# Kernel optimization log

Measured on AMD Instinct MI355X. Metric: run time of the kernel, lower is better.

## Reference

```python
import jax, jax.numpy as jnp
import numpy as np

HID = 1024
H = 8
HD = HID // H  # 128; KV length must equal HD for the bias-add broadcast
B = 8
LQ = 4096
LK = HD


def setup_inputs() -> dict:
    key = jax.random.key(0)
    ks = jax.random.split(key, 16)
    s = 0.02
    inp = {
        "query": jax.random.normal(ks[0], (B, LQ, HID), jnp.float32),
        "key": jax.random.normal(ks[1], (B, LK, HID), jnp.float32),
        "value": jax.random.normal(ks[2], (B, LK, HID), jnp.float32),
        "atten": jax.random.normal(ks[3], (B, LQ, HID), jnp.float32),
        "mask": jax.random.randint(ks[4], (B, 1, 1, LK), 0, 2, jnp.int32),
        "Wq": jax.random.normal(ks[5], (HID, HID), jnp.float32) * s,
        "bq": jnp.zeros((HID,), jnp.float32),
        "Wk": jax.random.normal(ks[6], (HID, HID), jnp.float32) * s,
        "bk": jnp.zeros((HID,), jnp.float32),
        "Wv": jax.random.normal(ks[7], (HID, HID), jnp.float32) * s,
        "bv": jnp.zeros((HID,), jnp.float32),
        "Watt": jax.random.normal(ks[8], (HID, HID), jnp.float32) * s,
        "batt": jnp.zeros((HID,), jnp.float32),
        "Wfc": jax.random.normal(ks[9], (HID, HID), jnp.float32) * s,
        "bfc": jnp.zeros((HID,), jnp.float32),
    }
    return inp


def _heads(x):
    # [B, L, HID] -> [B, H, L, HD]
    b, l, _ = x.shape
    return x.reshape(b, l, H, HD).transpose(0, 2, 1, 3)


def reference(query, key, value, atten, mask, Wq, bq, Wk, bk, Wv, bv, Watt, batt, Wfc, bfc):
    scale = jnp.sqrt(jnp.asarray(HD, jnp.float32))
    atten_out = _heads(atten @ Watt.T + batt)          # [B,H,LQ,HD]
    Q = _heads(query @ Wq.T + bq)                      # [B,H,LQ,HD]
    K = _heads(key @ Wk.T + bk)                        # [B,H,LK,HD]
    V = _heads(value @ Wv.T + bv)                      # [B,H,LK,HD]
    energy = jnp.einsum('bhqd,bhkd->bhqk', Q, K) / scale + atten_out  # LK == HD
    energy = jnp.where(mask == 0, jnp.float32(-1e10), energy)
    attention = jax.nn.softmax(energy, axis=-1)
    x = jnp.einsum('bhqk,bhkd->bhqd', attention, V)
    x = x.transpose(0, 2, 1, 3).reshape(query.shape[0], -1, HID)
    return x @ Wfc.T + bfc
```

## Files before the change

### kernel.cpp

```cpp
#include <hip/hip_runtime.h>
#include <hip/hip_bf16.h>
#include <stdint.h>

typedef __bf16 bf16_t;
typedef __bf16 bf16x8 __attribute__((ext_vector_type(8)));
typedef __bf16 bf16x4 __attribute__((ext_vector_type(4)));
typedef float f32x4 __attribute__((ext_vector_type(4)));

#define HIDN 1024
#define NHEAD 8
#define HDIM 128
#define NBATCH 8
#define LQLEN 4096
#define LKLEN 128

__device__ __forceinline__ void gload_lds16(const void* g, void* l) {
  __builtin_amdgcn_global_load_lds(
      (const __attribute__((address_space(1))) unsigned int*)g,
      (__attribute__((address_space(3))) unsigned int*)l, 16, 0, 0);
}

__global__ __launch_bounds__(256) void convk(const float* __restrict__ in,
                                             bf16_t* __restrict__ out, int n4) {
  int i = blockIdx.x * blockDim.x + threadIdx.x;
  const int stride = gridDim.x * blockDim.x;
  for (; i < n4; i += stride) {
    const float4 v = ((const float4*)in)[i];
    bf16x4 o;
    o[0] = (bf16_t)v.x; o[1] = (bf16_t)v.y; o[2] = (bf16_t)v.z; o[3] = (bf16_t)v.w;
    ((bf16x4*)out)[i] = o;
  }
}

template <int MODE>
__global__ __launch_bounds__(512, 2) void gemm8p(const bf16_t* __restrict__ A,
                                                 const bf16_t* __restrict__ Bw,
                                                 const float* __restrict__ bias,
                                                 void* __restrict__ Cout) {
  constexpr int NT = 32;
  constexpr int SLOT = 32768;
  __shared__ uint4 smem_raw[8192];
  char* smem = (char*)smem_raw;

  const int tid = threadIdx.x;
  const int wid = tid >> 6, lane = tid & 63;
  const int lr = lane & 15, lh = lane >> 4;
  const int wr = wid >> 2, wc = wid & 3;

  const int bid = blockIdx.x;
  const int m_blk = (bid & 7) * 16 + (bid >> 5);
  const int n_blk = (bid >> 3) & 3;
  const int m0 = m_blk * 256, n0 = n_blk * 256;

  const int c0 = tid, c1 = tid + 512;
  const int sc0 = (((c0 & 3) ^ ((c0 >> 3) & 3)) << 4);
  const int sc1 = (((c1 & 3) ^ ((c1 >> 3) & 3)) << 4);
  const char* srcA0 = (const char*)A + (size_t)(m0 + (c0 >> 2)) * 2048 + sc0;
  const char* srcA1 = (const char*)A + (size_t)(m0 + (c1 >> 2)) * 2048 + sc1;
  const char* srcB0 = (const char*)Bw + (size_t)(n0 + (c0 >> 2)) * 2048 + sc0;
  const char* srcB1 = (const char*)Bw + (size_t)(n0 + (c1 >> 2)) * 2048 + sc1;
  const int d0 = c0 * 16, d1 = c1 * 16;

  f32x4 acc[8][4] = {};

#pragma unroll
  for (int tt = 0; tt < 3; ++tt) {
    char* dst = smem + tt * SLOT;
    gload_lds16(srcA0 + tt * 64, dst + d0);
    gload_lds16(srcA1 + tt * 64, dst + d1);
    gload_lds16(srcB0 + tt * 64, dst + 16384 + d0);
    gload_lds16(srcB1 + tt * 64, dst + 16384 + d1);
  }
  asm volatile("s_waitcnt vmcnt(8)" ::: "memory");
  __builtin_amdgcn_s_barrier();
  __builtin_amdgcn_sched_barrier(0);

  const int swz = ((lr >> 1) & 3) << 4;
  const int aoff = (wr * 128 + lr) * 64 + ((lh << 4) ^ swz);
  const int boff = 16384 + (wc * 64 + lr) * 64 + ((lh << 4) ^ swz);

  for (int t = 0; t < NT; ++t) {
    const char* sA = smem + (t & 3) * SLOT + aoff;
    const char* sB = smem + (t & 3) * SLOT + boff;
    char* dst = smem + ((t + 3) & 3) * SLOT;
    const int kb = (t + 3) * 64;
    const bool pf = (t <= NT - 4);

    bf16x8 bfr[4], af[8];
#pragma unroll
    for (int n = 0; n < 4; ++n) bfr[n] = *(const bf16x8*)(sB + n * 1024);
#pragma unroll
    for (int m = 0; m < 8; ++m) af[m] = *(const bf16x8*)(sA + m * 1024);
    if (pf) {
      gload_lds16(srcA0 + kb, dst + d0);
      gload_lds16(srcA1 + kb, dst + d1);
      gload_lds16(srcB0 + kb, dst + 16384 + d0);
      gload_lds16(srcB1 + kb, dst + 16384 + d1);
    }
    __builtin_amdgcn_s_setprio(1);
#pragma unroll
    for (int m = 0; m < 8; ++m)
#pragma unroll
      for (int n = 0; n < 4; ++n)
        acc[m][n] = __builtin_amdgcn_mfma_f32_16x16x32_bf16(af[m], bfr[n], acc[m][n], 0, 0, 0);
    __builtin_amdgcn_s_setprio(0);

    if (t < NT - 1) {
      __builtin_amdgcn_sched_barrier(0);
      if (t <= NT - 4)
        asm volatile("s_waitcnt vmcnt(8)" ::: "memory");
      else if (t == NT - 3)
        asm volatile("s_waitcnt vmcnt(4)" ::: "memory");
      else
        asm volatile("s_waitcnt vmcnt(0)" ::: "memory");
      __builtin_amdgcn_s_barrier();
      __builtin_amdgcn_sched_barrier(0);
    }
  }

  if constexpr (MODE == 2) {
    float* C = (float*)Cout;
#pragma unroll
    for (int f = 0; f < 8; ++f) {
      const int gm = m0 + wr * 128 + f * 16 + lh * 4;
#pragma unroll
      for (int j = 0; j < 4; ++j) {
        const int gn = n0 + wc * 64 + j * 16 + lr;
        const float bb = bias[gn];
#pragma unroll
        for (int r = 0; r < 4; ++r)
          C[(size_t)(gm + r) * HIDN + gn] = acc[f][j][r] + bb;
      }
    }
  } else {
    __builtin_amdgcn_s_barrier();
    __builtin_amdgcn_sched_barrier(0);
    char* wlds = smem + wid * 16384;
#pragma unroll
    for (int f = 0; f < 8; ++f) {
#pragma unroll
      for (int j = 0; j < 4; ++j) {
        const int gn = n0 + wc * 64 + j * 16 + lr;
        const float bb = bias[gn];
#pragma unroll
        for (int r = 0; r < 4; ++r)
          *(bf16_t*)(wlds + (f * 16 + lh * 4 + r) * 128 + (j * 16 + lr) * 2) =
              (bf16_t)(acc[f][j][r] + bb);
      }
    }
    asm volatile("s_waitcnt lgkmcnt(0)" ::: "memory");
    __builtin_amdgcn_sched_barrier(0);
    bf16_t* C = (bf16_t*)Cout;
    const int gnb = n0 + wc * 64;
    const int h = gnb >> 7, dd = gnb & 127;
#pragma unroll
    for (int p = 0; p < 16; ++p) {
      const int rl = p * 8 + (lane >> 3);
      const int cb = (lane & 7) * 16;
      const uint4 v = *(const uint4*)(wlds + rl * 128 + cb);
      const int gm = m0 + wr * 128 + rl;
      const int b = gm >> 12, l = gm & 4095;
      char* dstp = (char*)(C + (((size_t)(b * NHEAD + h) * LQLEN + l) << 7) + dd) + cb;
      *(uint4*)dstp = v;
    }
  }
}

template <int MODE, int LROW>
__global__ __launch_bounds__(256) void gemm_bt(const bf16_t* __restrict__ A,
                                               const bf16_t* __restrict__ Bw,
                                               const float* __restrict__ bias,
                                               void* __restrict__ Cout) {
  constexpr int BK = 32;
  __shared__ uint4 AsRaw[128 * BK * 2 / 16];
  __shared__ uint4 BsRaw[128 * BK * 2 / 16];
  bf16_t* As = (bf16_t*)AsRaw;
  bf16_t* Bs = (bf16_t*)BsRaw;

  const int tid = threadIdx.x;
  const int wid = tid >> 6;
  const int lane = tid & 63;
  const int lr = lane & 15, lh = lane >> 4;
  const int m0 = blockIdx.x * 128, n0 = blockIdx.y * 128;
  const int wm = (wid >> 1) * 64, wn = (wid & 1) * 64;

  f32x4 acc[4][4] = {};

  const int srow = lane >> 2;
  const int scol = (lane & 3) * 16;

  for (int k0 = 0; k0 < HIDN; k0 += BK) {
#pragma unroll
    for (int i = 0; i < 2; ++i) {
      const int c = wid + i * 4;
      const int row = c * 16 + srow;
      gload_lds16((const char*)A + ((size_t)(m0 + row) * HIDN + k0) * 2 + scol,
                  (char*)As + c * 1024);
      gload_lds16((const char*)Bw + ((size_t)(n0 + row) * HIDN + k0) * 2 + scol,
                  (char*)Bs + c * 1024);
    }
    __syncthreads();

    bf16x8 af[4], bfr[4];
#pragma unroll
    for (int i = 0; i < 4; ++i) {
      af[i]  = *(const bf16x8*)(As + (wm + i * 16 + lr) * BK + lh * 8);
      bfr[i] = *(const bf16x8*)(Bs + (wn + i * 16 + lr) * BK + lh * 8);
    }
#pragma unroll
    for (int i = 0; i < 4; ++i)
#pragma unroll
      for (int j = 0; j < 4; ++j)
        acc[i][j] = __builtin_amdgcn_mfma_f32_16x16x32_bf16(af[i], bfr[j], acc[i][j], 0, 0, 0);
    __syncthreads();
  }

#pragma unroll
  for (int i = 0; i < 4; ++i) {
#pragma unroll
    for (int r = 0; r < 4; ++r) {
      const int gm = m0 + wm + i * 16 + lh * 4 + r;
#pragma unroll
      for (int j = 0; j < 4; ++j) {
        const int gn = n0 + wn + j * 16 + lr;
        const float v = acc[i][j][r] + bias[gn];
        const int b = gm / LROW, l = gm - b * LROW;
        const int h = gn >> 7, d = gn & 127;
        size_t idx;
        if constexpr (MODE == 0)
          idx = (((size_t)(b * NHEAD + h) * LROW + l) << 7) + d;
        else
          idx = (((size_t)(b * NHEAD + h) * 128 + d) << 7) + l;
        ((bf16_t*)Cout)[idx] = (bf16_t)v;
      }
    }
  }
}

__global__ __launch_bounds__(256) void attn_kernel(
    const bf16_t* __restrict__ Qh, const bf16_t* __restrict__ Ah,
    const bf16_t* __restrict__ Kh, const bf16_t* __restrict__ Vt,
    const int* __restrict__ mask, bf16_t* __restrict__ X) {
  __shared__ uint4 KsRaw[2048];
  __shared__ uint4 VsRaw[2048];
  __shared__ float Ms[128];
  char* Ks = (char*)KsRaw;
  char* Vs = (char*)VsRaw;

  const int tid = threadIdx.x, wid = tid >> 6, lane = tid & 63;
  const int lr = lane & 15, lh = lane >> 4;
  const int bh = blockIdx.y, b = bh >> 3, h = bh & 7;
  const int q0 = blockIdx.x * 64;

  {
    const char* Kg = (const char*)(Kh + (size_t)bh * 16384);
    const char* Vg = (const char*)(Vt + (size_t)bh * 16384);
#pragma unroll
    for (int it = 0; it < 8; ++it) {
      const int e = it * 256 + tid;
      const int row = e >> 4;
      const int cb = (e & 15) << 4;
      const int dst = row * 256 + (cb ^ ((row & 7) << 4));
      *(uint4*)(Ks + dst) = *(const uint4*)(Kg + row * 256 + cb);
      *(uint4*)(Vs + dst) = *(const uint4*)(Vg + row * 256 + cb);
    }
  }
  if (tid < 128) Ms[tid] = (mask[b * 128 + tid] == 0) ? 0.f : 1.f;

  bf16x8 qf[4];
  {
    const bf16_t* Qb = Qh + ((size_t)bh * LQLEN + q0 + wid * 16 + lr) * 128;
#pragma unroll
    for (int s = 0; s < 4; ++s) qf[s] = *(const bf16x8*)(Qb + s * 32 + lh * 8);
  }
  __syncthreads();

  f32x4 acc[8] = {};
#pragma unroll
  for (int nt = 0; nt < 8; ++nt) {
#pragma unroll
    for (int s = 0; s < 4; ++s) {
      const int row = nt * 16 + lr;
      const int cb = (s * 64 + lh * 16) ^ ((row & 7) << 4);
      const bf16x8 kf = *(const bf16x8*)(Ks + row * 256 + cb);
      acc[nt] = __builtin_amdgcn_mfma_f32_16x16x32_bf16(qf[s], kf, acc[nt], 0, 0, 0);
    }
  }

  float ex[8][4];
  float rsum[4];
  const float sc = 0.08838834764831845f;
  const bf16_t* Ab = Ah + ((size_t)bh * LQLEN + q0 + wid * 16) * 128;
#pragma unroll
  for (int r = 0; r < 4; ++r) {
    const int row = lh * 4 + r;
    float mx = -3.0e38f;
#pragma unroll
    for (int nt = 0; nt < 8; ++nt) {
      const int col = nt * 16 + lr;
      float e = acc[nt][r] * sc + (float)Ab[row * 128 + col];
      e = (Ms[col] != 0.f) ? e : -1.0e10f;
      ex[nt][r] = e;
      mx = fmaxf(mx, e);
    }
    mx = fmaxf(mx, __shfl_xor(mx, 1));
    mx = fmaxf(mx, __shfl_xor(mx, 2));
    mx = fmaxf(mx, __shfl_xor(mx, 4));
    mx = fmaxf(mx, __shfl_xor(mx, 8));
    float s_ = 0.f;
#pragma unroll
    for (int nt = 0; nt < 8; ++nt) {
      const float p = expf(ex[nt][r] - mx);
      ex[nt][r] = p;
      s_ += p;
    }
    s_ += __shfl_xor(s_, 1);
    s_ += __shfl_xor(s_, 2);
    s_ += __shfl_xor(s_, 4);
    s_ += __shfl_xor(s_, 8);
    rsum[r] = s_;
  }

  __syncthreads();
  char* Pb = Ks + wid * 4096;
#pragma unroll
  for (int r = 0; r < 4; ++r) {
    const int row = lh * 4 + r;
#pragma unroll
    for (int nt = 0; nt < 8; ++nt) {
      const int col = nt * 16 + lr;
      const int off = (row * 256 + col * 2) ^ ((row & 7) << 4);
      *(bf16_t*)(Pb + off) = (bf16_t)ex[nt][r];
    }
  }
  __syncthreads();

  bf16x8 pf[4];
#pragma unroll
  for (int s = 0; s < 4; ++s)
    pf[s] = *(const bf16x8*)(Pb + lr * 256 + ((s * 64 + lh * 16) ^ ((lr & 7) << 4)));
  f32x4 acc2[8] = {};
#pragma unroll
  for (int nt = 0; nt < 8; ++nt) {
#pragma unroll
    for (int s = 0; s < 4; ++s) {
      const int row = nt * 16 + lr;
      const int cb = (s * 64 + lh * 16) ^ ((row & 7) << 4);
      const bf16x8 vf = *(const bf16x8*)(Vs + row * 256 + cb);
      acc2[nt] = __builtin_amdgcn_mfma_f32_16x16x32_bf16(pf[s], vf, acc2[nt], 0, 0, 0);
    }
  }

  float rs[4];
#pragma unroll
  for (int r = 0; r < 4; ++r) rs[r] = 1.f / rsum[r];
  bf16_t* Xb = X + ((size_t)b * LQLEN + q0 + wid * 16) * HIDN + h * 128;
#pragma unroll
  for (int nt = 0; nt < 8; ++nt)
#pragma unroll
    for (int r = 0; r < 4; ++r)
      Xb[(size_t)(lh * 4 + r) * HIDN + nt * 16 + lr] = (bf16_t)(acc2[nt][r] * rs[r]);
}

extern "C" void kernel_launch(void* const* d_in, const int* in_sizes, int n_in,
                              void* d_out, int out_size, void* d_ws, size_t ws_size,
                              hipStream_t stream) {
  const float* query = (const float*)d_in[0];
  const float* key   = (const float*)d_in[1];
  const float* value = (const float*)d_in[2];
  const float* atten = (const float*)d_in[3];
  const int*   mask  = (const int*)d_in[4];
  const float* Wq  = (const float*)d_in[5];  const float* bq   = (const float*)d_in[6];
  const float* Wk  = (const float*)d_in[7];  const float* bk   = (const float*)d_in[8];
  const float* Wv  = (const float*)d_in[9];  const float* bv   = (const float*)d_in[10];
  const float* Wat = (const float*)d_in[11]; const float* batt = (const float*)d_in[12];
  const float* Wfc = (const float*)d_in[13]; const float* bfc  = (const float*)d_in[14];

  char* ws = (char*)d_ws;
  bf16_t* qbf = (bf16_t*)(ws + 0x0000000);
  bf16_t* abf = (bf16_t*)(ws + 0x4000000);
  bf16_t* Qh  = (bf16_t*)(ws + 0x8000000);
  bf16_t* Ah  = (bf16_t*)(ws + 0xC000000);
  char* sm = ws + 0x10000000;
  bf16_t* kbf = (bf16_t*)(sm + 0x000000);
  bf16_t* vbf = (bf16_t*)(sm + 0x200000);
  bf16_t* wqb = (bf16_t*)(sm + 0x400000);
  bf16_t* wkb = (bf16_t*)(sm + 0x600000);
  bf16_t* wvb = (bf16_t*)(sm + 0x800000);
  bf16_t* wab = (bf16_t*)(sm + 0xA00000);
  bf16_t* wfb = (bf16_t*)(sm + 0xC00000);
  bf16_t* Kh  = (bf16_t*)(sm + 0xE00000);
  bf16_t* Vt  = (bf16_t*)(sm + 0x1000000);
  bf16_t* X   = qbf;

  auto conv = [&](const float* src, bf16_t* dst, int n) {
    const int n4 = n >> 2;
    int g = (n4 + 255) >> 8; if (g > 2048) g = 2048;
    convk<<<dim3(g), dim3(256), 0, stream>>>(src, dst, n4);
  };
  conv(query, qbf, NBATCH * LQLEN * HIDN);
  conv(atten, abf, NBATCH * LQLEN * HIDN);
  conv(key,   kbf, NBATCH * LKLEN * HIDN);
  conv(value, vbf, NBATCH * LKLEN * HIDN);
  conv(Wq,  wqb, HIDN * HIDN);
  conv(Wk,  wkb, HIDN * HIDN);
  conv(Wv,  wvb, HIDN * HIDN);
  conv(Wat, wab, HIDN * HIDN);
  conv(Wfc, wfb, HIDN * HIDN);

  gemm_bt<0, 128><<<dim3(8, 8), dim3(256), 0, stream>>>(kbf, wkb, bk, (void*)Kh);
  gemm_bt<1, 128><<<dim3(8, 8), dim3(256), 0, stream>>>(vbf, wvb, bv, (void*)Vt);

  gemm8p<0><<<dim3(512), dim3(512), 0, stream>>>(qbf, wqb, bq, (void*)Qh);
  gemm8p<0><<<dim3(512), dim3(512), 0, stream>>>(abf, wab, batt, (void*)Ah);

  attn_kernel<<<dim3(LQLEN / 64, NBATCH * NHEAD), dim3(256), 0, stream>>>(
      Qh, Ah, Kh, Vt, mask, X);

  gemm8p<2><<<dim3(512), dim3(512), 0, stream>>>(X, wfb, bfc, d_out);
}
```

Before: 466.8 us.

## Retile GEMM to 256x128 with 3-stage ring, batch conversions, stage attention I/O via LDS

The main GEMM now uses 256-thread blocks with a 256x128 tile and a 3-slot LDS ring, moving from 4 slots and 8 waves to a 2x2 wave grid. This lowers LDS per block so more blocks fit per CU, but shortens the prefetch depth. The seven small fp32-to-bf16 conversions are merged into one launch to cut launch overhead. In the attention kernel, the atten tile is staged into LDS with async loads and the output is written through LDS as coalesced 16-byte stores, replacing scattered 2-byte global accesses at the cost of extra barriers.

Measured after the change: 473.4 us. About the same (+1.4%).

```diff
diff --git a/kernel.cpp b/kernel.cpp
--- a/kernel.cpp
+++ b/kernel.cpp
@@ -4,7 +4,6 @@
 
 typedef __bf16 bf16_t;
 typedef __bf16 bf16x8 __attribute__((ext_vector_type(8)));
-typedef __bf16 bf16x4 __attribute__((ext_vector_type(4)));
 typedef float f32x4 __attribute__((ext_vector_type(4)));
 
 #define HIDN 1024
@@ -26,52 +25,88 @@
   const int stride = gridDim.x * blockDim.x;
   for (; i < n4; i += stride) {
     const float4 v = ((const float4*)in)[i];
-    bf16x4 o;
+    bf16x8 o;
     o[0] = (bf16_t)v.x; o[1] = (bf16_t)v.y; o[2] = (bf16_t)v.z; o[3] = (bf16_t)v.w;
-    ((bf16x4*)out)[i] = o;
+    *(uint2*)((char*)out + (size_t)i * 8) = *(uint2*)&o;
+  }
+}
+
+__global__ __launch_bounds__(256) void convk7(
+    const float* s0, const float* s1, const float* s2, const float* s3,
+    const float* s4, const float* s5, const float* s6,
+    bf16_t* d0, bf16_t* d1, bf16_t* d2, bf16_t* d3,
+    bf16_t* d4, bf16_t* d5, bf16_t* d6) {
+  const float* src; bf16_t* dst;
+  switch (blockIdx.y) {
+    case 0: src = s0; dst = d0; break;
+    case 1: src = s1; dst = d1; break;
+    case 2: src = s2; dst = d2; break;
+    case 3: src = s3; dst = d3; break;
+    case 4: src = s4; dst = d4; break;
+    case 5: src = s5; dst = d5; break;
+    default: src = s6; dst = d6; break;
+  }
+  const int n4 = (1024 * 1024) / 4;
+  const int stride = gridDim.x * 256;
+  for (int i = blockIdx.x * 256 + threadIdx.x; i < n4; i += stride) {
+    const float4 v = ((const float4*)src)[i];
+    bf16x8 o;
+    o[0] = (bf16_t)v.x; o[1] = (bf16_t)v.y; o[2] = (bf16_t)v.z; o[3] = (bf16_t)v.w;
+    *(uint2*)((char*)dst + (size_t)i * 8) = *(uint2*)&o;
   }
 }
 
 template <int MODE>
-__global__ __launch_bounds__(512, 2) void gemm8p(const bf16_t* __restrict__ A,
+__global__ __launch_bounds__(256, 2) void gemm8p(const bf16_t* __restrict__ A,
                                                  const bf16_t* __restrict__ Bw,
                                                  const float* __restrict__ bias,
                                                  void* __restrict__ Cout) {
   constexpr int NT = 32;
-  constexpr int SLOT = 32768;
-  __shared__ uint4 smem_raw[8192];
+  constexpr int SLOT = 24576;
+  __shared__ uint4 smem_raw[4608];
   char* smem = (char*)smem_raw;
 
   const int tid = threadIdx.x;
   const int wid = tid >> 6, lane = tid & 63;
   const int lr = lane & 15, lh = lane >> 4;
-  const int wr = wid >> 2, wc = wid & 3;
+  const int wr = wid >> 1, wc = wid & 1;
 
   const int bid = blockIdx.x;
-  const int m_blk = (bid & 7) * 16 + (bid >> 5);
-  const int n_blk = (bid >> 3) & 3;
-  const int m0 = m_blk * 256, n0 = n_blk * 256;
-
-  const int c0 = tid, c1 = tid + 512;
-  const int sc0 = (((c0 & 3) ^ ((c0 >> 3) & 3)) << 4);
-  const int sc1 = (((c1 & 3) ^ ((c1 >> 3) & 3)) << 4);
-  const char* srcA0 = (const char*)A + (size_t)(m0 + (c0 >> 2)) * 2048 + sc0;
-  const char* srcA1 = (const char*)A + (size_t)(m0 + (c1 >> 2)) * 2048 + sc1;
-  const char* srcB0 = (const char*)Bw + (size_t)(n0 + (c0 >> 2)) * 2048 + sc0;
-  const char* srcB1 = (const char*)Bw + (size_t)(n0 + (c1 >> 2)) * 2048 + sc1;
-  const int d0 = c0 * 16, d1 = c1 * 16;
+  const int idx = bid >> 3;
+  const int n_blk = idx & 7;
+  const int m_blk = (bid & 7) * 16 + (idx >> 3);
+  const int m0 = m_blk * 256, n0 = n_blk * 128;
+
+  const char* srcA[4];
+  int dA[4];
+  const char* srcB[2];
+  int dB[2];
+#pragma unroll
+  for (int i = 0; i < 4; ++i) {
+    const int c = tid + 256 * i;
+    const int sl = (c & 3) ^ ((c >> 3) & 3);
+    srcA[i] = (const char*)A + (size_t)(m0 + (c >> 2)) * 2048 + (sl << 4);
+    dA[i] = c * 16;
+  }
+#pragma unroll
+  for (int i = 0; i < 2; ++i) {
+    const int c = tid + 256 * i;
+    const int sl = (c & 3) ^ ((c >> 3) & 3);
+    srcB[i] = (const char*)Bw + (size_t)(n0 + (c >> 2)) * 2048 + (sl << 4);
+    dB[i] = 16384 + c * 16;
+  }
 
   f32x4 acc[8][4] = {};
 
 #pragma unroll
   for (int tt = 0; tt < 3; ++tt) {
     char* dst = smem + tt * SLOT;
-    gload_lds16(srcA0 + tt * 64, dst + d0);
-    gload_lds16(srcA1 + tt * 64, dst + d1);
-    gload_lds16(srcB0 + tt * 64, dst + 16384 + d0);
-    gload_lds16(srcB1 + tt * 64, dst + 16384 + d1);
-  }
-  asm volatile("s_waitcnt vmcnt(8)" ::: "memory");
+#pragma unroll
+    for (int i = 0; i < 4; ++i) gload_lds16(srcA[i] + tt * 64, dst + dA[i]);
+#pragma unroll
+    for (int i = 0; i < 2; ++i) gload_lds16(srcB[i] + tt * 64, dst + dB[i]);
+  }
+  asm volatile("s_waitcnt vmcnt(12)" ::: "memory");
   __builtin_amdgcn_s_barrier();
   __builtin_amdgcn_sched_barrier(0);
 
@@ -79,24 +114,26 @@
   const int aoff = (wr * 128 + lr) * 64 + ((lh << 4) ^ swz);
   const int boff = 16384 + (wc * 64 + lr) * 64 + ((lh << 4) ^ swz);
 
+  int rs = 0, ss = 2;
   for (int t = 0; t < NT; ++t) {
-    const char* sA = smem + (t & 3) * SLOT + aoff;
-    const char* sB = smem + (t & 3) * SLOT + boff;
-    char* dst = smem + ((t + 3) & 3) * SLOT;
-    const int kb = (t + 3) * 64;
-    const bool pf = (t <= NT - 4);
+    const char* sA = smem + rs * SLOT + aoff;
+    const char* sB = smem + rs * SLOT + boff;
+
+    if (t <= NT - 3) {
+      char* dst = smem + ss * SLOT;
+      const int kb = (t + 2) * 64;
+#pragma unroll
+      for (int i = 0; i < 4; ++i) gload_lds16(srcA[i] + kb, dst + dA[i]);
+#pragma unroll
+      for (int i = 0; i < 2; ++i) gload_lds16(srcB[i] + kb, dst + dB[i]);
+    }
 
     bf16x8 bfr[4], af[8];
 #pragma unroll
     for (int n = 0; n < 4; ++n) bfr[n] = *(const bf16x8*)(sB + n * 1024);
 #pragma unroll
     for (int m = 0; m < 8; ++m) af[m] = *(const bf16x8*)(sA + m * 1024);
-    if (pf) {
-      gload_lds16(srcA0 + kb, dst + d0);
-      gload_lds16(srcA1 + kb, dst + d1);
-      gload_lds16(srcB0 + kb, dst + 16384 + d0);
-      gload_lds16(srcB1 + kb, dst + 16384 + d1);
-    }
+
     __builtin_amdgcn_s_setprio(1);
 #pragma unroll
     for (int m = 0; m < 8; ++m)
@@ -107,15 +144,16 @@
 
     if (t < NT - 1) {
       __builtin_amdgcn_sched_barrier(0);
-      if (t <= NT - 4)
-        asm volatile("s_waitcnt vmcnt(8)" ::: "memory");
-      else if (t == NT - 3)
-        asm volatile("s_waitcnt vmcnt(4)" ::: "memory");
+      if (t <= NT - 3)
+        asm volatile("s_waitcnt vmcnt(6)" ::: "memory");
       else
         asm volatile("s_waitcnt vmcnt(0)" ::: "memory");
+      __builtin_amdgcn_sched_barrier(0);
       __builtin_amdgcn_s_barrier();
       __builtin_amdgcn_sched_barrier(0);
     }
+    rs = (rs == 2) ? 0 : rs + 1;
+    ss = (ss == 2) ? 0 : ss + 1;
   }
 
   if constexpr (MODE == 2) {
@@ -286,19 +324,32 @@
       acc[nt] = __builtin_amdgcn_mfma_f32_16x16x32_bf16(qf[s], kf, acc[nt], 0, 0, 0);
     }
   }
+  __syncthreads();
+
+  {
+    const char* Ag = (const char*)(Ah + ((size_t)bh * LQLEN + q0) * 128);
+#pragma unroll
+    for (int it = 0; it < 4; ++it) {
+      const int c = it * 256 + tid;
+      gload_lds16(Ag + c * 16, Ks + 16384 + c * 16);
+    }
+  }
+  asm volatile("s_waitcnt vmcnt(0)" ::: "memory");
+  __syncthreads();
+  const char* Al = Ks + 16384;
 
   float ex[8][4];
   float rsum[4];
   const float sc = 0.08838834764831845f;
-  const bf16_t* Ab = Ah + ((size_t)bh * LQLEN + q0 + wid * 16) * 128;
 #pragma unroll
   for (int r = 0; r < 4; ++r) {
     const int row = lh * 4 + r;
+    const int rowg = wid * 16 + row;
     float mx = -3.0e38f;
 #pragma unroll
     for (int nt = 0; nt < 8; ++nt) {
       const int col = nt * 16 + lr;
-      float e = acc[nt][r] * sc + (float)Ab[row * 128 + col];
+      float e = acc[nt][r] * sc + (float)(*(const bf16_t*)(Al + rowg * 256 + col * 2));
       e = (Ms[col] != 0.f) ? e : -1.0e10f;
       ex[nt][r] = e;
       mx = fmaxf(mx, e);
@@ -321,7 +372,6 @@
     rsum[r] = s_;
   }
 
-  __syncthreads();
   char* Pb = Ks + wid * 4096;
 #pragma unroll
   for (int r = 0; r < 4; ++r) {
@@ -350,16 +400,29 @@
       acc2[nt] = __builtin_amdgcn_mfma_f32_16x16x32_bf16(pf[s], vf, acc2[nt], 0, 0, 0);
     }
   }
+  __syncthreads();
 
   float rs[4];
 #pragma unroll
   for (int r = 0; r < 4; ++r) rs[r] = 1.f / rsum[r];
-  bf16_t* Xb = X + ((size_t)b * LQLEN + q0 + wid * 16) * HIDN + h * 128;
 #pragma unroll
   for (int nt = 0; nt < 8; ++nt)
 #pragma unroll
     for (int r = 0; r < 4; ++r)
-      Xb[(size_t)(lh * 4 + r) * HIDN + nt * 16 + lr] = (bf16_t)(acc2[nt][r] * rs[r]);
+      *(bf16_t*)(Vs + (wid * 16 + lh * 4 + r) * 256 + (nt * 16 + lr) * 2) =
+          (bf16_t)(acc2[nt][r] * rs[r]);
+  asm volatile("s_waitcnt lgkmcnt(0)" ::: "memory");
+  __syncthreads();
+
+#pragma unroll
+  for (int it = 0; it < 4; ++it) {
+    const int c = it * 256 + tid;
+    const int row = c >> 4;
+    const int off = (c & 15) << 4;
+    const uint4 v = *(const uint4*)(Vs + row * 256 + off);
+    char* dstp = (char*)(X + ((size_t)(b * LQLEN) + q0 + row) * HIDN + h * 128) + off;
+    *(uint4*)dstp = v;
+  }
 }
 
 extern "C" void kernel_launch(void* const* d_in, const int* in_sizes, int n_in,
@@ -393,29 +456,20 @@
   bf16_t* Vt  = (bf16_t*)(sm + 0x1000000);
   bf16_t* X   = qbf;
 
-  auto conv = [&](const float* src, bf16_t* dst, int n) {
-    const int n4 = n >> 2;
-    int g = (n4 + 255) >> 8; if (g > 2048) g = 2048;
-    convk<<<dim3(g), dim3(256), 0, stream>>>(src, dst, n4);
-  };
-  conv(query, qbf, NBATCH * LQLEN * HIDN);
-  conv(atten, abf, NBATCH * LQLEN * HIDN);
-  conv(key,   kbf, NBATCH * LKLEN * HIDN);
-  conv(value, vbf, NBATCH * LKLEN * HIDN);
-  conv(Wq,  wqb, HIDN * HIDN);
-  conv(Wk,  wkb, HIDN * HIDN);
-  conv(Wv,  wvb, HIDN * HIDN);
-  conv(Wat, wab, HIDN * HIDN);
-  conv(Wfc, wfb, HIDN * HIDN);
+  convk7<<<dim3(256, 7), dim3(256), 0, stream>>>(
+      key, value, Wq, Wk, Wv, Wat, Wfc,
+      kbf, vbf, wqb, wkb, wvb, wab, wfb);
+  convk<<<dim3(2048), dim3(256), 0, stream>>>(query, qbf, NBATCH * LQLEN * HIDN / 4);
+  convk<<<dim3(2048), dim3(256), 0, stream>>>(atten, abf, NBATCH * LQLEN * HIDN / 4);
 
   gemm_bt<0, 128><<<dim3(8, 8), dim3(256), 0, stream>>>(kbf, wkb, bk, (void*)Kh);
   gemm_bt<1, 128><<<dim3(8, 8), dim3(256), 0, stream>>>(vbf, wvb, bv, (void*)Vt);
 
-  gemm8p<0><<<dim3(512), dim3(512), 0, stream>>>(qbf, wqb, bq, (void*)Qh);
-  gemm8p<0><<<dim3(512), dim3(512), 0, stream>>>(abf, wab, batt, (void*)Ah);
+  gemm8p<0><<<dim3(1024), dim3(256), 0, stream>>>(qbf, wqb, bq, (void*)Qh);
+  gemm8p<0><<<dim3(1024), dim3(256), 0, stream>>>(abf, wab, batt, (void*)Ah);
 
   attn_kernel<<<dim3(LQLEN / 64, NBATCH * NHEAD), dim3(256), 0, stream>>>(
       Qh, Ah, Kh, Vt, mask, X);
 
-  gemm8p<2><<<dim3(512), dim3(512), 0, stream>>>(X, wfb, bfc, d_out);
-}
+  gemm8p<2><<<dim3(1024), dim3(256), 0, stream>>>(X, wfb, bfc, d_out);
+}
```
